# Performance work log

Hardware: AMD Instinct MI355X
Metric: run time of the kernel (lower is better)

The kernel has to match this reference:

```python
import jax, jax.numpy as jnp
import numpy as np

EPS = 1.1920929e-07  # torch nn.RMSNorm default eps = finfo(fp32).eps
H, NOPE, ROPE, VD = 16, 128, 64, 128
QKD = NOPE + ROPE


def rmsnorm(x, w):
    return x * jax.lax.rsqrt(jnp.mean(x * x, axis=-1, keepdims=True) + EPS) * w


def rope(x, cos, sin):
    # x: [B,S,h,D]; cos/sin broadcast to [B,S,h,D//2]; pairs are (even, odd) interleaved
    x2 = x.reshape(*x.shape[:-1], -1, 2)
    x0, x1 = x2[..., 0], x2[..., 1]
    r = x0 * cos - x1 * sin
    i = x0 * sin + x1 * cos
    return jnp.stack([r, i], axis=-1).reshape(x.shape)


def setup_inputs() -> dict:
    key = jax.random.key(0)
    ks = jax.random.split(key, 8)
    B, S, D = 2, 2048, 2048
    QR, KR = 1536, 512
    x = jax.random.normal(ks[0], (B, S, D), jnp.float32)
    # RoPE table: theta=10000, rope dim 64 -> 32 frequencies
    pos = np.arange(S)[:, None]
    inv = 1.0 / (10000.0 ** (np.arange(0, ROPE, 2) / ROPE))[None, :]
    ang = pos * inv
    freqs_cos = jnp.asarray(np.cos(ang), jnp.float32)
    freqs_sin = jnp.asarray(np.sin(ang), jnp.float32)

    def w(k, out_dim, in_dim):
        return jax.random.normal(k, (out_dim, in_dim), jnp.float32) / np.sqrt(in_dim)

    return {
        "x": x,
        "freqs_cos": freqs_cos,
        "freqs_sin": freqs_sin,
        "Wq_down": w(ks[1], QR, D),
        "q_norm_w": jnp.ones((QR,), jnp.float32),
        "Wq_up": w(ks[2], H * QKD, QR),
        "Wkv_down": w(ks[3], ROPE + KR, D),
        "kv_norm_w": jnp.ones((KR,), jnp.float32),
        "Wkv_up": w(ks[4], H * (VD + NOPE), KR),
        "Wo": w(ks[5], D, H * VD),
        "bo": jnp.zeros((D,), jnp.float32),
        "start_pos": 0,
    }


def reference(x, freqs_cos, freqs_sin, Wq_down, q_norm_w, Wq_up, Wkv_down, kv_norm_w, Wkv_up, Wo, bo, start_pos):
    B, S, D = x.shape
    cos = freqs_cos[None, :, None, :]
    sin = freqs_sin[None, :, None, :]
    # low-rank Q path: down -> RMSNorm -> up
    q = rmsnorm(x @ Wq_down.T, q_norm_w) @ Wq_up.T
    q = q.reshape(B, S, H, QKD)
    q_nope, q_rope = q[..., :NOPE], q[..., NOPE:]
    q_rope = rope(q_rope, cos, sin)
    q = jnp.concatenate([q_nope, q_rope], axis=-1)  # [B,S,H,QKD]
    # low-rank KV path: shared rope part + latent kv
    kv = x @ Wkv_down.T
    k_rope, c_kv = kv[..., :ROPE], kv[..., ROPE:]
    k_rope = rope(k_rope[:, :, None, :], cos, sin)  # [B,S,1,ROPE]
    kv = rmsnorm(c_kv, kv_norm_w) @ Wkv_up.T
    kv = kv.reshape(B, S, H, NOPE + VD)
    k_nope, v = kv[..., :NOPE], kv[..., NOPE:]
    k = jnp.concatenate([k_nope, jnp.broadcast_to(k_rope, (B, S, H, ROPE))], axis=-1)
    # causal SDPA (start_pos=0 prefill: cache slice equals fresh K/V)
    scale = 1.0 / np.sqrt(QKD)
    scores = jnp.einsum("bqhd,bkhd->bhqk", q, k) * scale
    mask = jnp.tril(jnp.ones((S, S), bool))
    scores = jnp.where(mask, scores, -jnp.inf)
    attn = jax.nn.softmax(scores, axis=-1)
    o = jnp.einsum("bhqk,bkhd->bqhd", attn, v).reshape(B, S, H * VD)
    return o @ Wo.T + bo
```

## Files before the change

### kernel.cpp

```cpp
#include <hip/hip_runtime.h>
#include <hip/hip_bf16.h>
#include <stdint.h>


typedef short bf16x8 __attribute__((ext_vector_type(8)));
typedef float f32x4  __attribute__((ext_vector_type(4)));
typedef unsigned int u32;

#define RMS_EPS 1.1920929e-07f
#define SCALE_L2E 0.10411931095f

__device__ __forceinline__ unsigned short f2b(float f) {
  union { float f; uint32_t u; } c; c.f = f;
  uint32_t u = c.u;
  return (unsigned short)((u + 0x7FFFu + ((u >> 16) & 1u)) >> 16);
}
__device__ __forceinline__ float b2f(short s) {
  union { uint32_t u; float f; } c; c.u = ((uint32_t)(unsigned short)s) << 16;
  return c.f;
}
__device__ __forceinline__ u32 pk2(float a, float b) {
  union { __hip_bfloat162 h; u32 u; } cv;
  cv.h = __float22bfloat162_rn(float2{a, b});
  return cv.u;
// ... 143 lines not shown
        } else {
          o0 = v0; o1 = v1; o2 = v2; o3 = v3;
        }
        uint2 o;
        o.x = pk2(o0 * SCALE_L2E, o1 * SCALE_L2E);
        o.y = pk2(o2 * SCALE_L2E, o3 * SCALE_L2E);
        *(uint2*)(qb + ((size_t)((b * 16 + h) * 2048 + s)) * 192 + d0) = o;
      }
    }
  } else {
    short* kb = (short*)Cv;
    short* vT = aux;
    int h = col0 >> 8;
    if ((col0 & 128) == 0) {
#pragma unroll
      for (int j = 0; j < 4; ++j) {
        int d = wn * 64 + j * 16 + l15;
#pragma unroll
        for (int i = 0; i < 4; ++i) {
          int rowb = row0 + wm * 64 + i * 16 + l4 * 4;
#pragma unroll
          for (int r = 0; r < 4; ++r) {
            int row = rowb + r;
            int b = row >> 11, s = row & 2047;
            kb[((size_t)((b * 16 + h) * 2048 + s)) * 128 + d] = (short)f2b(acc[i][j][r]);
          }
        }
      }
    } else {
#pragma unroll
      for (int j = 0; j < 4; ++j) {
        int dv = wn * 64 + j * 16 + l15;
#pragma unroll
        for (int i = 0; i < 4; ++i) {
          int s0 = row0 + wm * 64 + i * 16 + l4 * 4;
          int b = s0 >> 11, s = s0 & 2047;
          short4 o;
          o.x = (short)f2b(acc[i][j][0]);
          o.y = (short)f2b(acc[i][j][1]);
          o.z = (short)f2b(acc[i][j][2]);
          o.w = (short)f2b(acc[i][j][3]);
          *(short4*)(vT + ((size_t)((b * 16 + h) * 128 + dv)) * 2048 + s) = o;
        }
      }
    }
  }
}

template <int EPI>
__global__ __launch_bounds__(256) void gemm_bt(
    const short* __restrict__ A, const short* __restrict__ Bt,
    void* __restrict__ Cv, const float* __restrict__ bias,
    int K, int ldc,
    const float* __restrict__ fc, const float* __restrict__ fs,
    short* __restrict__ aux) {
  __shared__ __align__(16) short As[128 * 64];
  __shared__ __align__(16) short Bs[128 * 64];
  int nx = gridDim.x;
  int lin = blockIdx.y * nx + blockIdx.x;
  int cpx = (nx * gridDim.y) >> 3;
  int swz = (lin & 7) * cpx + (lin >> 3);
  int row0 = (swz / nx) * 128, col0 = (swz % nx) * 128;
  gemm_body<EPI>(As, Bs, row0, col0, A, Bt, Cv, bias, K, ldc, fc, fs, aux);
}

__global__ __launch_bounds__(256) void gemm_up(
    const short* __restrict__ qn, const short* __restrict__ wqu,
    short* __restrict__ q_b,
    const short* __restrict__ ckvn, const short* __restrict__ wkvu,
    short* __restrict__ k_b, short* __restrict__ vT,
    const float* __restrict__ fc, const float* __restrict__ fs) {
  __shared__ __align__(16) short As[128 * 64];
  __shared__ __align__(16) short Bs[128 * 64];
  int bb = blockIdx.x;
  if (bb < 768) {
    int cpx = 768 >> 3;
    int swz = (bb & 7) * cpx + (bb >> 3);
    int row0 = (swz / 24) * 128, col0 = (swz % 24) * 128;
    gemm_body<2>(As, Bs, row0, col0, qn, wqu, q_b, nullptr, 1536, 0, fc, fs, nullptr);
  } else {
    int bb2 = bb - 768;
    int cpx = 1024 >> 3;
    int swz = (bb2 & 7) * cpx + (bb2 >> 3);
    int row0 = (swz / 32) * 128, col0 = (swz % 32) * 128;
    gemm_body<3>(As, Bs, row0, col0, ckvn, wkvu, k_b, nullptr, 512, 0, nullptr, nullptr, vT);
  }
}

template <int W>
__device__ __forceinline__ void rms_body(
    const short* __restrict__ in, const float* __restrict__ wgt,
    short* __restrict__ out, int ld_in, int blk) {
  constexpr int NC = W / 512;
  int row = blk * 4 + (threadIdx.x >> 6);
  int lane = threadIdx.x & 63;
  const short* x = in + (size_t)row * ld_in + lane * 8;
  float vals[NC * 8];
  float ss = 0.f;
#pragma unroll
  for (int c = 0; c < NC; ++c) {
    bf16x8 v = *(const bf16x8*)(x + c * 512);
#pragma unroll
    for (int k = 0; k < 8; ++k) {
      float f = b2f(v[k]);
      vals[c * 8 + k] = f; ss += f * f;
    }
  }
#pragma unroll
  for (int off = 32; off > 0; off >>= 1) ss += __shfl_xor(ss, off);
  float rs = rsqrtf(ss / (float)W + RMS_EPS);
  short* o = out + (size_t)row * W + lane * 8;
#pragma unroll
  for (int c = 0; c < NC; ++c) {
    const float4* wp = (const float4*)(wgt + c * 512 + lane * 8);
    float4 w0 = wp[0], w1 = wp[1];
    ushort4 lo, hi;
    lo.x = f2b(vals[c * 8 + 0] * rs * w0.x);
    lo.y = f2b(vals[c * 8 + 1] * rs * w0.y);
    lo.z = f2b(vals[c * 8 + 2] * rs * w0.z);
    lo.w = f2b(vals[c * 8 + 3] * rs * w0.w);
    hi.x = f2b(vals[c * 8 + 4] * rs * w1.x);
    hi.y = f2b(vals[c * 8 + 5] * rs * w1.y);
    hi.z = f2b(vals[c * 8 + 6] * rs * w1.z);
    hi.w = f2b(vals[c * 8 + 7] * rs * w1.w);
    *(ushort4*)(o + c * 512) = lo;
    *(ushort4*)(o + c * 512 + 4) = hi;
  }
}

__global__ __launch_bounds__(256) void norm_krope_kernel(
    const short* __restrict__ c1,
    const float* __restrict__ qnw, short* __restrict__ qn,
    const float* __restrict__ kvnw, short* __restrict__ ckvn,
    const float* __restrict__ fc, const float* __restrict__ fs,
    short* __restrict__ kr) {
  int bb = blockIdx.x;
  if (bb < 1024) {
    rms_body<1536>(c1, qnw, qn, 2176, bb);
  } else if (bb < 2048) {
    rms_body<512>(c1 + 1600, kvnw, ckvn, 2176, bb - 1024);
  } else {
    int idx = (bb - 2048) * 256 + threadIdx.x;
    int i = idx & 31;
    int s = (idx >> 5) & 2047;
    int b = idx >> 16;
    const short* row = c1 + (size_t)(b * 2048 + s) * 2176 + 1536 + 2 * i;
    float x0 = b2f(row[0]), x1 = b2f(row[1]);
    float c = fc[s * 32 + i], sn = fs[s * 32 + i];
    uint32_t pk = (uint32_t)f2b(x0 * c - x1 * sn) | ((uint32_t)f2b(x0 * sn + x1 * c) << 16);
    *(uint32_t*)(kr + ((size_t)(b * 2048 + s)) * 64 + 2 * i) = pk;
  }
}

__global__ __launch_bounds__(256, 2) void attn_kernel(
    const short* __restrict__ qb, const short* __restrict__ kb,
    const short* __restrict__ kr, const short* __restrict__ vtb,
    short* __restrict__ ob) {
  __shared__ __align__(16) short Ks[64 * 196];
  __shared__ __align__(16) short Vs[128 * 70];
  int bid = blockIdx.x;
  int xcd = bid & 7, kk2 = bid >> 3;
  int bh = xcd * 4 + (kk2 >> 4);
  int qx = kk2 & 15;
  int b = bh >> 4, h = bh & 15;
  int t = threadIdx.x, lane = t & 63, w = t >> 6;
  int l15 = lane & 15, l4 = lane >> 4;
  const short* Kbh = kb + (size_t)bh * 2048 * 128;
  const short* krb = kr + (size_t)b * 2048 * 64;
  const short* Vbh = vtb + (size_t)bh * 128 * 2048;

  int kn_r = t >> 4, kn_c = (t & 15) * 8;
  int kr_r = t >> 3, kr_c = (t & 7) * 8;
  int v_d = t >> 3, v_c = (t & 7) * 8;

  int sA = (l15 + ((l4 & 1) << 5)) << 2;
  int sB = sA + (16 << 2);
  bool chi = (l4 >> 1) != 0;

  for (int half = 0; half < 2; ++half) {
    int qt = half ? (31 - qx) : qx;
    int q0 = qt * 64;
    const short* Qbase = qb + ((size_t)bh * 2048 + q0 + w * 16) * 192;
    bf16x8 qf[6];
#pragma unroll
    for (int kk = 0; kk < 6; ++kk)
      qf[kk] = *(const bf16x8*)(Qbase + (size_t)l15 * 192 + kk * 32 + l4 * 8);
    f32x4 oaccT[8] = {};
    float m_i = -1e30f, l_i = 0.f;
    int qcol = q0 + w * 16 + l15;
    int kend = q0 + 64;

    bf16x8 pn0, pn1, pn2, pn3, pr0, pr1, pv0, pv1, pv2, pv3;
    pn0 = *(const bf16x8*)(Kbh + (size_t)(kn_r) * 128 + kn_c);
    pn1 = *(const bf16x8*)(Kbh + (size_t)(kn_r + 16) * 128 + kn_c);
    pn2 = *(const bf16x8*)(Kbh + (size_t)(kn_r + 32) * 128 + kn_c);
    pn3 = *(const bf16x8*)(Kbh + (size_t)(kn_r + 48) * 128 + kn_c);
    pr0 = *(const bf16x8*)(krb + (size_t)(kr_r) * 64 + kr_c);
    pr1 = *(const bf16x8*)(krb + (size_t)(kr_r + 32) * 64 + kr_c);
    pv0 = *(const bf16x8*)(Vbh + (size_t)(v_d) * 2048 + v_c);
    pv1 = *(const bf16x8*)(Vbh + (size_t)(v_d + 32) * 2048 + v_c);
    pv2 = *(const bf16x8*)(Vbh + (size_t)(v_d + 64) * 2048 + v_c);
    pv3 = *(const bf16x8*)(Vbh + (size_t)(v_d + 96) * 2048 + v_c);

    for (int kt = 0; kt < kend; kt += 64) {
      *(bf16x8*)(Ks + (kn_r) * 196 + kn_c) = pn0;
      *(bf16x8*)(Ks + (kn_r + 16) * 196 + kn_c) = pn1;
      *(bf16x8*)(Ks + (kn_r + 32) * 196 + kn_c) = pn2;
      *(bf16x8*)(Ks + (kn_r + 48) * 196 + kn_c) = pn3;
      *(bf16x8*)(Ks + (kr_r) * 196 + 128 + kr_c) = pr0;
      *(bf16x8*)(Ks + (kr_r + 32) * 196 + 128 + kr_c) = pr1;
      *(bf16x8*)(Vs + (v_d) * 70 + v_c) = pv0;
      *(bf16x8*)(Vs + (v_d + 32) * 70 + v_c) = pv1;
      *(bf16x8*)(Vs + (v_d + 64) * 70 + v_c) = pv2;
      *(bf16x8*)(Vs + (v_d + 96) * 70 + v_c) = pv3;
      __syncthreads();
      if (kt + 64 < kend) {
        int k2 = kt + 64;
        pn0 = *(const bf16x8*)(Kbh + (size_t)(k2 + kn_r) * 128 + kn_c);
        pn1 = *(const bf16x8*)(Kbh + (size_t)(k2 + kn_r + 16) * 128 + kn_c);
        pn2 = *(const bf16x8*)(Kbh + (size_t)(k2 + kn_r + 32) * 128 + kn_c);
        pn3 = *(const bf16x8*)(Kbh + (size_t)(k2 + kn_r + 48) * 128 + kn_c);
        pr0 = *(const bf16x8*)(krb + (size_t)(k2 + kr_r) * 64 + kr_c);
        pr1 = *(const bf16x8*)(krb + (size_t)(k2 + kr_r + 32) * 64 + kr_c);
        pv0 = *(const bf16x8*)(Vbh + (size_t)(v_d) * 2048 + k2 + v_c);
        pv1 = *(const bf16x8*)(Vbh + (size_t)(v_d + 32) * 2048 + k2 + v_c);
        pv2 = *(const bf16x8*)(Vbh + (size_t)(v_d + 64) * 2048 + k2 + v_c);
        pv3 = *(const bf16x8*)(Vbh + (size_t)(v_d + 96) * 2048 + k2 + v_c);
      }

      f32x4 s[4] = {};
      __builtin_amdgcn_s_setprio(1);
#pragma unroll
      for (int kk = 0; kk < 6; ++kk) {
#pragma unroll
        for (int c = 0; c < 4; ++c) {
          bf16x8 kf = *(const bf16x8*)(Ks + (c * 16 + l15) * 196 + kk * 32 + l4 * 8);
          s[c] = __builtin_amdgcn_mfma_f32_16x16x32_bf16(kf, qf[kk], s[c], 0, 0, 0);
        }
      }
      __builtin_amdgcn_s_setprio(0);

      if (kt == q0) {
#pragma unroll
        for (int c = 0; c < 4; ++c)
#pragma unroll
          for (int r = 0; r < 4; ++r) {
            int k = kt + c * 16 + l4 * 4 + r;
            if (k > qcol) s[c][r] = -1e30f;
          }
      }
      float mx = fmaxf(fmaxf(fmaxf(s[0][0], s[0][1]), fmaxf(s[0][2], s[0][3])),
                       fmaxf(fmaxf(s[1][0], s[1][1]), fmaxf(s[1][2], s[1][3])));
      mx = fmaxf(mx, fmaxf(fmaxf(fmaxf(s[2][0], s[2][1]), fmaxf(s[2][2], s[2][3])),
                           fmaxf(fmaxf(s[3][0], s[3][1]), fmaxf(s[3][2], s[3][3]))));
      mx = fmaxf(mx, __shfl_xor(mx, 16));
      mx = fmaxf(mx, __shfl_xor(mx, 32));
      float newm = fmaxf(m_i, mx);
      float alpha = __builtin_amdgcn_exp2f(m_i - newm);
      float rs = 0.f;
#pragma unroll
      for (int c = 0; c < 4; ++c)
#pragma unroll
        for (int r = 0; r < 4; ++r) {
          float p = __builtin_amdgcn_exp2f(s[c][r] - newm);
          s[c][r] = p; rs += p;
        }
      rs += __shfl_xor(rs, 16);
      rs += __shfl_xor(rs, 32);
      l_i = l_i * alpha + rs;
      m_i = newm;
#pragma unroll
      for (int dt = 0; dt < 8; ++dt)
#pragma unroll
        for (int r = 0; r < 4; ++r) oaccT[dt][r] *= alpha;

      u32 pk00 = pk2(s[0][0], s[0][1]), pk01 = pk2(s[0][2], s[0][3]);
      u32 pk10 = pk2(s[1][0], s[1][1]), pk11 = pk2(s[1][2], s[1][3]);
      u32 pk20 = pk2(s[2][0], s[2][1]), pk21 = pk2(s[2][2], s[2][3]);
      u32 pk30 = pk2(s[3][0], s[3][1]), pk31 = pk2(s[3][2], s[3][3]);
      union { bf16x8 v; u32 u[4]; } P0, P1;
      {
        u32 a0 = __builtin_amdgcn_ds_bpermute(sA, (int)pk00);
        u32 a1 = __builtin_amdgcn_ds_bpermute(sA, (int)pk01);
        u32 a2 = __builtin_amdgcn_ds_bpermute(sB, (int)pk00);
        u32 a3 = __builtin_amdgcn_ds_bpermute(sB, (int)pk01);
        u32 b0 = __builtin_amdgcn_ds_bpermute(sA, (int)pk10);
        u32 b1 = __builtin_amdgcn_ds_bpermute(sA, (int)pk11);
        u32 b2 = __builtin_amdgcn_ds_bpermute(sB, (int)pk10);
        u32 b3 = __builtin_amdgcn_ds_bpermute(sB, (int)pk11);
        P0.u[0] = chi ? b0 : a0; P0.u[1] = chi ? b1 : a1;
        P0.u[2] = chi ? b2 : a2; P0.u[3] = chi ? b3 : a3;
      }
      {
        u32 a0 = __builtin_amdgcn_ds_bpermute(sA, (int)pk20);
        u32 a1 = __builtin_amdgcn_ds_bpermute(sA, (int)pk21);
        u32 a2 = __builtin_amdgcn_ds_bpermute(sB, (int)pk20);
        u32 a3 = __builtin_amdgcn_ds_bpermute(sB, (int)pk21);
        u32 b0 = __builtin_amdgcn_ds_bpermute(sA, (int)pk30);
        u32 b1 = __builtin_amdgcn_ds_bpermute(sA, (int)pk31);
        u32 b2 = __builtin_amdgcn_ds_bpermute(sB, (int)pk30);
        u32 b3 = __builtin_amdgcn_ds_bpermute(sB, (int)pk31);
        P1.u[0] = chi ? b0 : a0; P1.u[1] = chi ? b1 : a1;
        P1.u[2] = chi ? b2 : a2; P1.u[3] = chi ? b3 : a3;
      }

      __builtin_amdgcn_s_setprio(1);
#pragma unroll
      for (int dt = 0; dt < 8; ++dt) {
        bf16x8 vf0 = *(const bf16x8*)(Vs + (dt * 16 + l15) * 70 + l4 * 8);
        bf16x8 vf1 = *(const bf16x8*)(Vs + (dt * 16 + l15) * 70 + 32 + l4 * 8);
        oaccT[dt] = __builtin_amdgcn_mfma_f32_16x16x32_bf16(vf0, P0.v, oaccT[dt], 0, 0, 0);
        oaccT[dt] = __builtin_amdgcn_mfma_f32_16x16x32_bf16(vf1, P1.v, oaccT[dt], 0, 0, 0);
      }
      __builtin_amdgcn_s_setprio(0);
      __syncthreads();
    }
    float inv = 1.0f / l_i;
    short* dst = ob + ((size_t)(b * 2048 + qcol)) * 2048 + h * 128;
#pragma unroll
    for (int dt = 0; dt < 8; ++dt) {
      uint2 o;
      o.x = pk2(oaccT[dt][0] * inv, oaccT[dt][1] * inv);
      o.y = pk2(oaccT[dt][2] * inv, oaccT[dt][3] * inv);
      *(uint2*)(dst + dt * 16 + l4 * 4) = o;
    }
  }
}

extern "C" void kernel_launch(void* const* d_in, const int* in_sizes, int n_in,
                              void* d_out, int out_size, void* d_ws, size_t ws_size,
                              hipStream_t stream) {
  const float* x    = (const float*)d_in[0];
  const float* fcos = (const float*)d_in[1];
  const float* fsin = (const float*)d_in[2];
  const float* Wqd  = (const float*)d_in[3];
  const float* qnw  = (const float*)d_in[4];
  const float* Wqu  = (const float*)d_in[5];
  const float* Wkvd = (const float*)d_in[6];
  const float* kvnw = (const float*)d_in[7];
  const float* Wkvu = (const float*)d_in[8];
  const float* Wo   = (const float*)d_in[9];
  const float* bo   = (const float*)d_in[10];
  float* out = (float*)d_out;
  char* ws = (char*)d_ws;

  short* x_bf  = (short*)(ws + 0);
  short* w_cat = (short*)(ws + 16777216);
  short* w_qu  = (short*)(ws + 25690112);
  short* w_kvu = (short*)(ws + 35127296);
  short* w_o   = (short*)(ws + 39321600);
  short* c1    = (short*)(ws + 47710208);
  short* qn    = (short*)(ws + 65536000);
  short* ckvn  = (short*)(ws + 78118912);
  short* q_b   = (short*)(ws + 82313216);
  short* k_b   = (short*)(ws + 107479040);
  short* vT    = (short*)(ws + 132644864);
  short* o_bf  = (short*)(ws + 149422080);
  short* kr    = (short*)(ws + 166199296);

  f2bf_all_kernel<<<23296, 256, 0, stream>>>(x, x_bf, Wqd, w_cat, Wqu, w_qu,
                                             Wkvu, w_kvu, Wo, w_o,
                                             Wkvd, w_cat + 1536 * 2048);

  gemm_bt<1><<<dim3(17, 32), 256, 0, stream>>>(x_bf, w_cat, c1, nullptr, 2048, 2176,
                                               nullptr, nullptr, nullptr);
  norm_krope_kernel<<<2560, 256, 0, stream>>>(c1, qnw, qn, kvnw, ckvn,
                                              fcos, fsin, kr);

  gemm_up<<<1792, 256, 0, stream>>>(qn, w_qu, q_b, ckvn, w_kvu, k_b, vT,
                                    fcos, fsin);

  attn_kernel<<<512, 256, 0, stream>>>(q_b, k_b, kr, vT, o_bf);

  gemm_bt<0><<<dim3(16, 32), 256, 0, stream>>>(o_bf, w_o, out, bo, 2048, 2048,
                                               nullptr, nullptr, nullptr);
}
```

Baseline: 336.6 us.

## Split attention KV range across two blocks with a separate combine kernel

Each query-tile pair is now handled by two blocks, each covering half of the causal KV range and writing an unnormalized bf16 partial output along with its running max and sum. A new combine kernel merges the two partials with log-sum-exp weights and writes the normalized output. This doubles the attention grid to 1024 blocks to improve CU occupancy and load balance. It costs an extra kernel launch, extra global traffic for the partials, and some precision loss from storing unnormalized partials in bf16.

```diff
diff --git a/kernel.cpp b/kernel.cpp
--- a/kernel.cpp
+++ b/kernel.cpp
@@ -322,18 +322,18 @@
 __global__ __launch_bounds__(256, 2) void attn_kernel(
     const short* __restrict__ qb, const short* __restrict__ kb,
     const short* __restrict__ kr, const short* __restrict__ vtb,
-    short* __restrict__ ob) {
+    short* __restrict__ po, float* __restrict__ pml) {
   __shared__ __align__(16) short Ks[64 * 196];
   __shared__ __align__(16) short Vs[128 * 70];
   int bid = blockIdx.x;
-  int xcd = bid & 7, kk2 = bid >> 3;
-  int bh = xcd * 4 + (kk2 >> 4);
-  int qx = kk2 & 15;
-  int b = bh >> 4, h = bh & 15;
+  int xcd = bid & 7, rest = bid >> 3;
+  int bh = xcd * 4 + (rest >> 5);
+  int idx = rest & 31;
+  int p = idx >> 1, j = idx & 1;
   int t = threadIdx.x, lane = t & 63, w = t >> 6;
   int l15 = lane & 15, l4 = lane >> 4;
   const short* Kbh = kb + (size_t)bh * 2048 * 128;
-  const short* krb = kr + (size_t)b * 2048 * 64;
+  const short* krb = kr + (size_t)(bh >> 4) * 2048 * 64;
   const short* Vbh = vtb + (size_t)bh * 128 * 2048;
 
   int kn_r = t >> 4, kn_c = (t & 15) * 8;
@@ -345,8 +345,11 @@
   bool chi = (l4 >> 1) != 0;
 
   for (int half = 0; half < 2; ++half) {
-    int qt = half ? (31 - qx) : qx;
+    int qt = half ? (31 - p) : p;
     int q0 = qt * 64;
+    int n = qt + 1;
+    int lo = j * ((n + 1) >> 1);
+    int hi = j ? n : ((n + 1) >> 1);
     const short* Qbase = qb + ((size_t)bh * 2048 + q0 + w * 16) * 192;
     bf16x8 qf[6];
 #pragma unroll
@@ -355,142 +358,181 @@
     f32x4 oaccT[8] = {};
     float m_i = -1e30f, l_i = 0.f;
     int qcol = q0 + w * 16 + l15;
-    int kend = q0 + 64;
-
-    bf16x8 pn0, pn1, pn2, pn3, pr0, pr1, pv0, pv1, pv2, pv3;
-    pn0 = *(const bf16x8*)(Kbh + (size_t)(kn_r) * 128 + kn_c);
-    pn1 = *(const bf16x8*)(Kbh + (size_t)(kn_r + 16) * 128 + kn_c);
-    pn2 = *(const bf16x8*)(Kbh + (size_t)(kn_r + 32) * 128 + kn_c);
-    pn3 = *(const bf16x8*)(Kbh + (size_t)(kn_r + 48) * 128 + kn_c);
-    pr0 = *(const bf16x8*)(krb + (size_t)(kr_r) * 64 + kr_c);
-    pr1 = *(const bf16x8*)(krb + (size_t)(kr_r + 32) * 64 + kr_c);
-    pv0 = *(const bf16x8*)(Vbh + (size_t)(v_d) * 2048 + v_c);
-    pv1 = *(const bf16x8*)(Vbh + (size_t)(v_d + 32) * 2048 + v_c);
-    pv2 = *(const bf16x8*)(Vbh + (size_t)(v_d + 64) * 2048 + v_c);
-    pv3 = *(const bf16x8*)(Vbh + (size_t)(v_d + 96) * 2048 + v_c);
-
-    for (int kt = 0; kt < kend; kt += 64) {
-      *(bf16x8*)(Ks + (kn_r) * 196 + kn_c) = pn0;
-      *(bf16x8*)(Ks + (kn_r + 16) * 196 + kn_c) = pn1;
-      *(bf16x8*)(Ks + (kn_r + 32) * 196 + kn_c) = pn2;
-      *(bf16x8*)(Ks + (kn_r + 48) * 196 + kn_c) = pn3;
-      *(bf16x8*)(Ks + (kr_r) * 196 + 128 + kr_c) = pr0;
-      *(bf16x8*)(Ks + (kr_r + 32) * 196 + 128 + kr_c) = pr1;
-      *(bf16x8*)(Vs + (v_d) * 70 + v_c) = pv0;
-      *(bf16x8*)(Vs + (v_d + 32) * 70 + v_c) = pv1;
-      *(bf16x8*)(Vs + (v_d + 64) * 70 + v_c) = pv2;
-      *(bf16x8*)(Vs + (v_d + 96) * 70 + v_c) = pv3;
-      __syncthreads();
-      if (kt + 64 < kend) {
-        int k2 = kt + 64;
-        pn0 = *(const bf16x8*)(Kbh + (size_t)(k2 + kn_r) * 128 + kn_c);
-        pn1 = *(const bf16x8*)(Kbh + (size_t)(k2 + kn_r + 16) * 128 + kn_c);
-        pn2 = *(const bf16x8*)(Kbh + (size_t)(k2 + kn_r + 32) * 128 + kn_c);
-        pn3 = *(const bf16x8*)(Kbh + (size_t)(k2 + kn_r + 48) * 128 + kn_c);
-        pr0 = *(const bf16x8*)(krb + (size_t)(k2 + kr_r) * 64 + kr_c);
-        pr1 = *(const bf16x8*)(krb + (size_t)(k2 + kr_r + 32) * 64 + kr_c);
-        pv0 = *(const bf16x8*)(Vbh + (size_t)(v_d) * 2048 + k2 + v_c);
-        pv1 = *(const bf16x8*)(Vbh + (size_t)(v_d + 32) * 2048 + k2 + v_c);
-        pv2 = *(const bf16x8*)(Vbh + (size_t)(v_d + 64) * 2048 + k2 + v_c);
-        pv3 = *(const bf16x8*)(Vbh + (size_t)(v_d + 96) * 2048 + k2 + v_c);
-      }
-
-      f32x4 s[4] = {};
-      __builtin_amdgcn_s_setprio(1);
-#pragma unroll
-      for (int kk = 0; kk < 6; ++kk) {
-#pragma unroll
-        for (int c = 0; c < 4; ++c) {
-          bf16x8 kf = *(const bf16x8*)(Ks + (c * 16 + l15) * 196 + kk * 32 + l4 * 8);
-          s[c] = __builtin_amdgcn_mfma_f32_16x16x32_bf16(kf, qf[kk], s[c], 0, 0, 0);
-        }
-      }
-      __builtin_amdgcn_s_setprio(0);
-
-      if (kt == q0) {
+
+    if (lo < hi) {
+      bf16x8 pn0, pn1, pn2, pn3, pr0, pr1, pv0, pv1, pv2, pv3;
+      int k0 = lo * 64;
+      pn0 = *(const bf16x8*)(Kbh + (size_t)(k0 + kn_r) * 128 + kn_c);
+      pn1 = *(const bf16x8*)(Kbh + (size_t)(k0 + kn_r + 16) * 128 + kn_c);
+      pn2 = *(const bf16x8*)(Kbh + (size_t)(k0 + kn_r + 32) * 128 + kn_c);
+      pn3 = *(const bf16x8*)(Kbh + (size_t)(k0 + kn_r + 48) * 128 + kn_c);
+      pr0 = *(const bf16x8*)(krb + (size_t)(k0 + kr_r) * 64 + kr_c);
+      pr1 = *(const bf16x8*)(krb + (size_t)(k0 + kr_r + 32) * 64 + kr_c);
+      pv0 = *(const bf16x8*)(Vbh + (size_t)(v_d) * 2048 + k0 + v_c);
+      pv1 = *(const bf16x8*)(Vbh + (size_t)(v_d + 32) * 2048 + k0 + v_c);
+      pv2 = *(const bf16x8*)(Vbh + (size_t)(v_d + 64) * 2048 + k0 + v_c);
+      pv3 = *(const bf16x8*)(Vbh + (size_t)(v_d + 96) * 2048 + k0 + v_c);
+
+      for (int kt = lo * 64; kt < hi * 64; kt += 64) {
+        *(bf16x8*)(Ks + (kn_r) * 196 + kn_c) = pn0;
+        *(bf16x8*)(Ks + (kn_r + 16) * 196 + kn_c) = pn1;
+        *(bf16x8*)(Ks + (kn_r + 32) * 196 + kn_c) = pn2;
+        *(bf16x8*)(Ks + (kn_r + 48) * 196 + kn_c) = pn3;
+        *(bf16x8*)(Ks + (kr_r) * 196 + 128 + kr_c) = pr0;
+        *(bf16x8*)(Ks + (kr_r + 32) * 196 + 128 + kr_c) = pr1;
+        *(bf16x8*)(Vs + (v_d) * 70 + v_c) = pv0;
+        *(bf16x8*)(Vs + (v_d + 32) * 70 + v_c) = pv1;
+        *(bf16x8*)(Vs + (v_d + 64) * 70 + v_c) = pv2;
+        *(bf16x8*)(Vs + (v_d + 96) * 70 + v_c) = pv3;
+        __syncthreads();
+        if (kt + 64 < hi * 64) {
+          int k2 = kt + 64;
+          pn0 = *(const bf16x8*)(Kbh + (size_t)(k2 + kn_r) * 128 + kn_c);
+          pn1 = *(const bf16x8*)(Kbh + (size_t)(k2 + kn_r + 16) * 128 + kn_c);
+          pn2 = *(const bf16x8*)(Kbh + (size_t)(k2 + kn_r + 32) * 128 + kn_c);
+          pn3 = *(const bf16x8*)(Kbh + (size_t)(k2 + kn_r + 48) * 128 + kn_c);
+          pr0 = *(const bf16x8*)(krb + (size_t)(k2 + kr_r) * 64 + kr_c);
+          pr1 = *(const bf16x8*)(krb + (size_t)(k2 + kr_r + 32) * 64 + kr_c);
+          pv0 = *(const bf16x8*)(Vbh + (size_t)(v_d) * 2048 + k2 + v_c);
+          pv1 = *(const bf16x8*)(Vbh + (size_t)(v_d + 32) * 2048 + k2 + v_c);
+          pv2 = *(const bf16x8*)(Vbh + (size_t)(v_d + 64) * 2048 + k2 + v_c);
+          pv3 = *(const bf16x8*)(Vbh + (size_t)(v_d + 96) * 2048 + k2 + v_c);
+        }
+
+        f32x4 s[4] = {};
+        __builtin_amdgcn_s_setprio(1);
+#pragma unroll
+        for (int kk = 0; kk < 6; ++kk) {
+#pragma unroll
+          for (int c = 0; c < 4; ++c) {
+            bf16x8 kf = *(const bf16x8*)(Ks + (c * 16 + l15) * 196 + kk * 32 + l4 * 8);
+            s[c] = __builtin_amdgcn_mfma_f32_16x16x32_bf16(kf, qf[kk], s[c], 0, 0, 0);
+          }
+        }
+        __builtin_amdgcn_s_setprio(0);
+
+        if (kt == q0) {
+#pragma unroll
+          for (int c = 0; c < 4; ++c)
+#pragma unroll
+            for (int r = 0; r < 4; ++r) {
+              int k = kt + c * 16 + l4 * 4 + r;
+              if (k > qcol) s[c][r] = -1e30f;
+            }
+        }
+        float mx = fmaxf(fmaxf(fmaxf(s[0][0], s[0][1]), fmaxf(s[0][2], s[0][3])),
+                         fmaxf(fmaxf(s[1][0], s[1][1]), fmaxf(s[1][2], s[1][3])));
+        mx = fmaxf(mx, fmaxf(fmaxf(fmaxf(s[2][0], s[2][1]), fmaxf(s[2][2], s[2][3])),
+                             fmaxf(fmaxf(s[3][0], s[3][1]), fmaxf(s[3][2], s[3][3]))));
+        mx = fmaxf(mx, __shfl_xor(mx, 16));
+        mx = fmaxf(mx, __shfl_xor(mx, 32));
+        float newm = fmaxf(m_i, mx);
+        float alpha = __builtin_amdgcn_exp2f(m_i - newm);
+        float rs = 0.f;
 #pragma unroll
         for (int c = 0; c < 4; ++c)
 #pragma unroll
           for (int r = 0; r < 4; ++r) {
-            int k = kt + c * 16 + l4 * 4 + r;
-            if (k > qcol) s[c][r] = -1e30f;
+            float pv = __builtin_amdgcn_exp2f(s[c][r] - newm);
+            s[c][r] = pv; rs += pv;
           }
-      }
-      float mx = fmaxf(fmaxf(fmaxf(s[0][0], s[0][1]), fmaxf(s[0][2], s[0][3])),
-                       fmaxf(fmaxf(s[1][0], s[1][1]), fmaxf(s[1][2], s[1][3])));
-      mx = fmaxf(mx, fmaxf(fmaxf(fmaxf(s[2][0], s[2][1]), fmaxf(s[2][2], s[2][3])),
-                           fmaxf(fmaxf(s[3][0], s[3][1]), fmaxf(s[3][2], s[3][3]))));
-      mx = fmaxf(mx, __shfl_xor(mx, 16));
-      mx = fmaxf(mx, __shfl_xor(mx, 32));
-      float newm = fmaxf(m_i, mx);
-      float alpha = __builtin_amdgcn_exp2f(m_i - newm);
-      float rs = 0.f;
-#pragma unroll
-      for (int c = 0; c < 4; ++c)
-#pragma unroll
-        for (int r = 0; r < 4; ++r) {
-          float p = __builtin_amdgcn_exp2f(s[c][r] - newm);
-          s[c][r] = p; rs += p;
-        }
-      rs += __shfl_xor(rs, 16);
-      rs += __shfl_xor(rs, 32);
-      l_i = l_i * alpha + rs;
-      m_i = newm;
-#pragma unroll
-      for (int dt = 0; dt < 8; ++dt)
-#pragma unroll
-        for (int r = 0; r < 4; ++r) oaccT[dt][r] *= alpha;
-
-      u32 pk00 = pk2(s[0][0], s[0][1]), pk01 = pk2(s[0][2], s[0][3]);
-      u32 pk10 = pk2(s[1][0], s[1][1]), pk11 = pk2(s[1][2], s[1][3]);
-      u32 pk20 = pk2(s[2][0], s[2][1]), pk21 = pk2(s[2][2], s[2][3]);
-      u32 pk30 = pk2(s[3][0], s[3][1]), pk31 = pk2(s[3][2], s[3][3]);
-      union { bf16x8 v; u32 u[4]; } P0, P1;
-      {
-        u32 a0 = __builtin_amdgcn_ds_bpermute(sA, (int)pk00);
-        u32 a1 = __builtin_amdgcn_ds_bpermute(sA, (int)pk01);
-        u32 a2 = __builtin_amdgcn_ds_bpermute(sB, (int)pk00);
-        u32 a3 = __builtin_amdgcn_ds_bpermute(sB, (int)pk01);
-        u32 b0 = __builtin_amdgcn_ds_bpermute(sA, (int)pk10);
-        u32 b1 = __builtin_amdgcn_ds_bpermute(sA, (int)pk11);
-        u32 b2 = __builtin_amdgcn_ds_bpermute(sB, (int)pk10);
-        u32 b3 = __builtin_amdgcn_ds_bpermute(sB, (int)pk11);
-        P0.u[0] = chi ? b0 : a0; P0.u[1] = chi ? b1 : a1;
-        P0.u[2] = chi ? b2 : a2; P0.u[3] = chi ? b3 : a3;
-      }
-      {
-        u32 a0 = __builtin_amdgcn_ds_bpermute(sA, (int)pk20);
-        u32 a1 = __builtin_amdgcn_ds_bpermute(sA, (int)pk21);
-        u32 a2 = __builtin_amdgcn_ds_bpermute(sB, (int)pk20);
-        u32 a3 = __builtin_amdgcn_ds_bpermute(sB, (int)pk21);
-        u32 b0 = __builtin_amdgcn_ds_bpermute(sA, (int)pk30);
-        u32 b1 = __builtin_amdgcn_ds_bpermute(sA, (int)pk31);
-        u32 b2 = __builtin_amdgcn_ds_bpermute(sB, (int)pk30);
-        u32 b3 = __builtin_amdgcn_ds_bpermute(sB, (int)pk31);
-        P1.u[0] = chi ? b0 : a0; P1.u[1] = chi ? b1 : a1;
-        P1.u[2] = chi ? b2 : a2; P1.u[3] = chi ? b3 : a3;
-      }
-
-      __builtin_amdgcn_s_setprio(1);
-#pragma unroll
-      for (int dt = 0; dt < 8; ++dt) {
-        bf16x8 vf0 = *(const bf16x8*)(Vs + (dt * 16 + l15) * 70 + l4 * 8);
-        bf16x8 vf1 = *(const bf16x8*)(Vs + (dt * 16 + l15) * 70 + 32 + l4 * 8);
-        oaccT[dt] = __builtin_amdgcn_mfma_f32_16x16x32_bf16(vf0, P0.v, oaccT[dt], 0, 0, 0);
-        oaccT[dt] = __builtin_amdgcn_mfma_f32_16x16x32_bf16(vf1, P1.v, oaccT[dt], 0, 0, 0);
-      }
-      __builtin_amdgcn_s_setprio(0);
-      __syncthreads();
-    }
-    float inv = 1.0f / l_i;
-    short* dst = ob + ((size_t)(b * 2048 + qcol)) * 2048 + h * 128;
+        rs += __shfl_xor(rs, 16);
+        rs += __shfl_xor(rs, 32);
+        l_i = l_i * alpha + rs;
+        m_i = newm;
+#pragma unroll
+        for (int dt = 0; dt < 8; ++dt)
+#pragma unroll
+          for (int r = 0; r < 4; ++r) oaccT[dt][r] *= alpha;
+
+        u32 pk00 = pk2(s[0][0], s[0][1]), pk01 = pk2(s[0][2], s[0][3]);
+        u32 pk10 = pk2(s[1][0], s[1][1]), pk11 = pk2(s[1][2], s[1][3]);
+        u32 pk20 = pk2(s[2][0], s[2][1]), pk21 = pk2(s[2][2], s[2][3]);
+        u32 pk30 = pk2(s[3][0], s[3][1]), pk31 = pk2(s[3][2], s[3][3]);
+        union { bf16x8 v; u32 u[4]; } P0, P1;
+        {
+          u32 a0 = __builtin_amdgcn_ds_bpermute(sA, (int)pk00);
+          u32 a1 = __builtin_amdgcn_ds_bpermute(sA, (int)pk01);
+          u32 a2 = __builtin_amdgcn_ds_bpermute(sB, (int)pk00);
+          u32 a3 = __builtin_amdgcn_ds_bpermute(sB, (int)pk01);
+          u32 b0 = __builtin_amdgcn_ds_bpermute(sA, (int)pk10);
+          u32 b1 = __builtin_amdgcn_ds_bpermute(sA, (int)pk11);
+          u32 b2 = __builtin_amdgcn_ds_bpermute(sB, (int)pk10);
+          u32 b3 = __builtin_amdgcn_ds_bpermute(sB, (int)pk11);
+          P0.u[0] = chi ? b0 : a0; P0.u[1] = chi ? b1 : a1;
+          P0.u[2] = chi ? b2 : a2; P0.u[3] = chi ? b3 : a3;
+        }
+        {
+          u32 a0 = __builtin_amdgcn_ds_bpermute(sA, (int)pk20);
+          u32 a1 = __builtin_amdgcn_ds_bpermute(sA, (int)pk21);
+          u32 a2 = __builtin_amdgcn_ds_bpermute(sB, (int)pk20);
+          u32 a3 = __builtin_amdgcn_ds_bpermute(sB, (int)pk21);
+          u32 b0 = __builtin_amdgcn_ds_bpermute(sA, (int)pk30);
+          u32 b1 = __builtin_amdgcn_ds_bpermute(sA, (int)pk31);
+          u32 b2 = __builtin_amdgcn_ds_bpermute(sB, (int)pk30);
+          u32 b3 = __builtin_amdgcn_ds_bpermute(sB, (int)pk31);
+          P1.u[0] = chi ? b0 : a0; P1.u[1] = chi ? b1 : a1;
+          P1.u[2] = chi ? b2 : a2; P1.u[3] = chi ? b3 : a3;
+        }
+
+        __builtin_amdgcn_s_setprio(1);
+#pragma unroll
+        for (int dt = 0; dt < 8; ++dt) {
+          bf16x8 vf0 = *(const bf16x8*)(Vs + (dt * 16 + l15) * 70 + l4 * 8);
+          bf16x8 vf1 = *(const bf16x8*)(Vs + (dt * 16 + l15) * 70 + 32 + l4 * 8);
+          oaccT[dt] = __builtin_amdgcn_mfma_f32_16x16x32_bf16(vf0, P0.v, oaccT[dt], 0, 0, 0);
+          oaccT[dt] = __builtin_amdgcn_mfma_f32_16x16x32_bf16(vf1, P1.v, oaccT[dt], 0, 0, 0);
+        }
+        __builtin_amdgcn_s_setprio(0);
+        __syncthreads();
+      }
+    }
+    size_t pidx = ((size_t)bh * 32 + qt) * 2 + j;
+    short* dst = po + pidx * 8192 + (size_t)(w * 16 + l15) * 128;
 #pragma unroll
     for (int dt = 0; dt < 8; ++dt) {
       uint2 o;
-      o.x = pk2(oaccT[dt][0] * inv, oaccT[dt][1] * inv);
-      o.y = pk2(oaccT[dt][2] * inv, oaccT[dt][3] * inv);
+      o.x = pk2(oaccT[dt][0], oaccT[dt][1]);
+      o.y = pk2(oaccT[dt][2], oaccT[dt][3]);
       *(uint2*)(dst + dt * 16 + l4 * 4) = o;
     }
+    if (l4 == 0) {
+      float2 ml = {m_i, l_i};
+      *(float2*)(pml + pidx * 128 + (w * 16 + l15) * 2) = ml;
+    }
+  }
+}
+
+__global__ __launch_bounds__(256) void attn_combine_kernel(
+    const short* __restrict__ po, const float* __restrict__ pml,
+    short* __restrict__ ob) {
+  int bid = blockIdx.x;
+  int bh = bid >> 5, qt = bid & 31;
+  int b = bh >> 4, h = bh & 15;
+  int t = threadIdx.x;
+  int q = t >> 2, ds = (t & 3) * 32;
+  const float* ml0 = pml + ((size_t)bid * 2) * 128 + q * 2;
+  const float* ml1 = ml0 + 128;
+  float m0 = ml0[0], l0v = ml0[1];
+  float m1 = ml1[0], l1v = ml1[1];
+  float mm = fmaxf(m0, m1);
+  float w0 = __builtin_amdgcn_exp2f(m0 - mm);
+  float w1 = __builtin_amdgcn_exp2f(m1 - mm);
+  float inv = 1.0f / (l0v * w0 + l1v * w1);
+  w0 *= inv; w1 *= inv;
+  const short* p0 = po + ((size_t)bid * 2) * 8192 + q * 128 + ds;
+  const short* p1 = p0 + 8192;
+  short* dst = ob + ((size_t)(b * 2048 + qt * 64 + q)) * 2048 + h * 128 + ds;
+#pragma unroll
+  for (int c = 0; c < 4; ++c) {
+    bf16x8 a = *(const bf16x8*)(p0 + c * 8);
+    bf16x8 bb = *(const bf16x8*)(p1 + c * 8);
+    union { bf16x8 v; u32 u[4]; } o;
+    o.u[0] = pk2(b2f(a[0]) * w0 + b2f(bb[0]) * w1, b2f(a[1]) * w0 + b2f(bb[1]) * w1);
+    o.u[1] = pk2(b2f(a[2]) * w0 + b2f(bb[2]) * w1, b2f(a[3]) * w0 + b2f(bb[3]) * w1);
+    o.u[2] = pk2(b2f(a[4]) * w0 + b2f(bb[4]) * w1, b2f(a[5]) * w0 + b2f(bb[5]) * w1);
+    o.u[3] = pk2(b2f(a[6]) * w0 + b2f(bb[6]) * w1, b2f(a[7]) * w0 + b2f(bb[7]) * w1);
+    *(bf16x8*)(dst + c * 8) = o.v;
   }
 }
 
@@ -524,6 +566,8 @@
   short* vT    = (short*)(ws + 132644864);
   short* o_bf  = (short*)(ws + 149422080);
   short* kr    = (short*)(ws + 166199296);
+  short* po    = (short*)(ws + 166723584);
+  float* pml   = (float*)(ws + 200278016);
 
   f2bf_all_kernel<<<23296, 256, 0, stream>>>(x, x_bf, Wqd, w_cat, Wqu, w_qu,
                                              Wkvu, w_kvu, Wo, w_o,
@@ -537,7 +581,8 @@
   gemm_up<<<1792, 256, 0, stream>>>(qn, w_qu, q_b, ckvn, w_kvu, k_b, vT,
                                     fcos, fsin);
 
-  attn_kernel<<<512, 256, 0, stream>>>(q_b, k_b, kr, vT, o_bf);
+  attn_kernel<<<1024, 256, 0, stream>>>(q_b, k_b, kr, vT, po, pml);
+  attn_combine_kernel<<<1024, 256, 0, stream>>>(po, pml, o_bf);
 
   gemm_bt<0><<<dim3(16, 32), 256, 0, stream>>>(o_bf, w_o, out, bo, 2048, 2048,
                                                nullptr, nullptr, nullptr);
```

Result: slower. 356.7 us (+6.0%).

## Share K/V tile loads between paired causal query tiles in attention

Applied to the files above, without the earlier changes.

The attention kernel used to process its two query tiles (qx and 31-qx) one after another, streaming K/V from global memory once per tile. It now keeps both tiles' Q fragments and accumulators live at the same time and walks K/V only once. Each staged tile feeds the long query tile, and also the short one while it is still inside its causal range. This roughly halves K/V global loads and barrier rounds per block, but doubles the accumulator and Q register footprint, which risks spills or lower occupancy under launch_bounds(256,2).

```diff
diff --git a/kernel.cpp b/kernel.cpp
--- a/kernel.cpp
+++ b/kernel.cpp
@@ -319,6 +319,97 @@
   }
 }
 
+__device__ __forceinline__ void attn_step(
+    const short* Ks, const short* Vs, const bf16x8 (&qf)[6],
+    f32x4 (&oaccT)[8], float& m_i, float& l_i,
+    int kt, int q0, int qcol, int l15, int l4, int sA, int sB, bool chi) {
+  f32x4 s[4] = {};
+  __builtin_amdgcn_s_setprio(1);
+#pragma unroll
+  for (int kk = 0; kk < 6; ++kk) {
+#pragma unroll
+    for (int c = 0; c < 4; ++c) {
+      bf16x8 kf = *(const bf16x8*)(Ks + (c * 16 + l15) * 196 + kk * 32 + l4 * 8);
+      s[c] = __builtin_amdgcn_mfma_f32_16x16x32_bf16(kf, qf[kk], s[c], 0, 0, 0);
+    }
+  }
+  __builtin_amdgcn_s_setprio(0);
+
+  if (kt == q0) {
+#pragma unroll
+    for (int c = 0; c < 4; ++c)
+#pragma unroll
+      for (int r = 0; r < 4; ++r) {
+        int k = kt + c * 16 + l4 * 4 + r;
+        if (k > qcol) s[c][r] = -1e30f;
+      }
+  }
+  float mx = fmaxf(fmaxf(fmaxf(s[0][0], s[0][1]), fmaxf(s[0][2], s[0][3])),
+                   fmaxf(fmaxf(s[1][0], s[1][1]), fmaxf(s[1][2], s[1][3])));
+  mx = fmaxf(mx, fmaxf(fmaxf(fmaxf(s[2][0], s[2][1]), fmaxf(s[2][2], s[2][3])),
+                       fmaxf(fmaxf(s[3][0], s[3][1]), fmaxf(s[3][2], s[3][3]))));
+  mx = fmaxf(mx, __shfl_xor(mx, 16));
+  mx = fmaxf(mx, __shfl_xor(mx, 32));
+  float newm = fmaxf(m_i, mx);
+  float alpha = __builtin_amdgcn_exp2f(m_i - newm);
+  float rs = 0.f;
+#pragma unroll
+  for (int c = 0; c < 4; ++c)
+#pragma unroll
+    for (int r = 0; r < 4; ++r) {
+      float p = __builtin_amdgcn_exp2f(s[c][r] - newm);
+      s[c][r] = p; rs += p;
+    }
+  rs += __shfl_xor(rs, 16);
+  rs += __shfl_xor(rs, 32);
+  l_i = l_i * alpha + rs;
+  m_i = newm;
+#pragma unroll
+  for (int dt = 0; dt < 8; ++dt)
+#pragma unroll
+    for (int r = 0; r < 4; ++r) oaccT[dt][r] *= alpha;
+
+  u32 pk00 = pk2(s[0][0], s[0][1]), pk01 = pk2(s[0][2], s[0][3]);
+  u32 pk10 = pk2(s[1][0], s[1][1]), pk11 = pk2(s[1][2], s[1][3]);
+  u32 pk20 = pk2(s[2][0], s[2][1]), pk21 = pk2(s[2][2], s[2][3]);
+  u32 pk30 = pk2(s[3][0], s[3][1]), pk31 = pk2(s[3][2], s[3][3]);
+  union { bf16x8 v; u32 u[4]; } P0, P1;
+  {
+    u32 a0 = __builtin_amdgcn_ds_bpermute(sA, (int)pk00);
+    u32 a1 = __builtin_amdgcn_ds_bpermute(sA, (int)pk01);
+    u32 a2 = __builtin_amdgcn_ds_bpermute(sB, (int)pk00);
+    u32 a3 = __builtin_amdgcn_ds_bpermute(sB, (int)pk01);
+    u32 b0 = __builtin_amdgcn_ds_bpermute(sA, (int)pk10);
+    u32 b1 = __builtin_amdgcn_ds_bpermute(sA, (int)pk11);
+    u32 b2 = __builtin_amdgcn_ds_bpermute(sB, (int)pk10);
+    u32 b3 = __builtin_amdgcn_ds_bpermute(sB, (int)pk11);
+    P0.u[0] = chi ? b0 : a0; P0.u[1] = chi ? b1 : a1;
+    P0.u[2] = chi ? b2 : a2; P0.u[3] = chi ? b3 : a3;
+  }
+  {
+    u32 a0 = __builtin_amdgcn_ds_bpermute(sA, (int)pk20);
+    u32 a1 = __builtin_amdgcn_ds_bpermute(sA, (int)pk21);
+    u32 a2 = __builtin_amdgcn_ds_bpermute(sB, (int)pk20);
+    u32 a3 = __builtin_amdgcn_ds_bpermute(sB, (int)pk21);
+    u32 b0 = __builtin_amdgcn_ds_bpermute(sA, (int)pk30);
+    u32 b1 = __builtin_amdgcn_ds_bpermute(sA, (int)pk31);
+    u32 b2 = __builtin_amdgcn_ds_bpermute(sB, (int)pk30);
+    u32 b3 = __builtin_amdgcn_ds_bpermute(sB, (int)pk31);
+    P1.u[0] = chi ? b0 : a0; P1.u[1] = chi ? b1 : a1;
+    P1.u[2] = chi ? b2 : a2; P1.u[3] = chi ? b3 : a3;
+  }
+
+  __builtin_amdgcn_s_setprio(1);
+#pragma unroll
+  for (int dt = 0; dt < 8; ++dt) {
+    bf16x8 vf0 = *(const bf16x8*)(Vs + (dt * 16 + l15) * 70 + l4 * 8);
+    bf16x8 vf1 = *(const bf16x8*)(Vs + (dt * 16 + l15) * 70 + 32 + l4 * 8);
+    oaccT[dt] = __builtin_amdgcn_mfma_f32_16x16x32_bf16(vf0, P0.v, oaccT[dt], 0, 0, 0);
+    oaccT[dt] = __builtin_amdgcn_mfma_f32_16x16x32_bf16(vf1, P1.v, oaccT[dt], 0, 0, 0);
+  }
+  __builtin_amdgcn_s_setprio(0);
+}
+
 __global__ __launch_bounds__(256, 2) void attn_kernel(
     const short* __restrict__ qb, const short* __restrict__ kb,
     const short* __restrict__ kr, const short* __restrict__ vtb,
@@ -344,153 +435,78 @@
   int sB = sA + (16 << 2);
   bool chi = (l4 >> 1) != 0;
 
-  for (int half = 0; half < 2; ++half) {
-    int qt = half ? (31 - qx) : qx;
-    int q0 = qt * 64;
-    const short* Qbase = qb + ((size_t)bh * 2048 + q0 + w * 16) * 192;
-    bf16x8 qf[6];
-#pragma unroll
-    for (int kk = 0; kk < 6; ++kk)
-      qf[kk] = *(const bf16x8*)(Qbase + (size_t)l15 * 192 + kk * 32 + l4 * 8);
-    f32x4 oaccT[8] = {};
-    float m_i = -1e30f, l_i = 0.f;
-    int qcol = q0 + w * 16 + l15;
-    int kend = q0 + 64;
-
-    bf16x8 pn0, pn1, pn2, pn3, pr0, pr1, pv0, pv1, pv2, pv3;
-    pn0 = *(const bf16x8*)(Kbh + (size_t)(kn_r) * 128 + kn_c);
-    pn1 = *(const bf16x8*)(Kbh + (size_t)(kn_r + 16) * 128 + kn_c);
-    pn2 = *(const bf16x8*)(Kbh + (size_t)(kn_r + 32) * 128 + kn_c);
-    pn3 = *(const bf16x8*)(Kbh + (size_t)(kn_r + 48) * 128 + kn_c);
-    pr0 = *(const bf16x8*)(krb + (size_t)(kr_r) * 64 + kr_c);
-    pr1 = *(const bf16x8*)(krb + (size_t)(kr_r + 32) * 64 + kr_c);
-    pv0 = *(const bf16x8*)(Vbh + (size_t)(v_d) * 2048 + v_c);
-    pv1 = *(const bf16x8*)(Vbh + (size_t)(v_d + 32) * 2048 + v_c);
-    pv2 = *(const bf16x8*)(Vbh + (size_t)(v_d + 64) * 2048 + v_c);
-    pv3 = *(const bf16x8*)(Vbh + (size_t)(v_d + 96) * 2048 + v_c);
-
-    for (int kt = 0; kt < kend; kt += 64) {
-      *(bf16x8*)(Ks + (kn_r) * 196 + kn_c) = pn0;
-      *(bf16x8*)(Ks + (kn_r + 16) * 196 + kn_c) = pn1;
-      *(bf16x8*)(Ks + (kn_r + 32) * 196 + kn_c) = pn2;
-      *(bf16x8*)(Ks + (kn_r + 48) * 196 + kn_c) = pn3;
-      *(bf16x8*)(Ks + (kr_r) * 196 + 128 + kr_c) = pr0;
-      *(bf16x8*)(Ks + (kr_r + 32) * 196 + 128 + kr_c) = pr1;
-      *(bf16x8*)(Vs + (v_d) * 70 + v_c) = pv0;
-      *(bf16x8*)(Vs + (v_d + 32) * 70 + v_c) = pv1;
-      *(bf16x8*)(Vs + (v_d + 64) * 70 + v_c) = pv2;
-      *(bf16x8*)(Vs + (v_d + 96) * 70 + v_c) = pv3;
-      __syncthreads();
-      if (kt + 64 < kend) {
-        int k2 = kt + 64;
-        pn0 = *(const bf16x8*)(Kbh + (size_t)(k2 + kn_r) * 128 + kn_c);
-        pn1 = *(const bf16x8*)(Kbh + (size_t)(k2 + kn_r + 16) * 128 + kn_c);
-        pn2 = *(const bf16x8*)(Kbh + (size_t)(k2 + kn_r + 32) * 128 + kn_c);
-        pn3 = *(const bf16x8*)(Kbh + (size_t)(k2 + kn_r + 48) * 128 + kn_c);
-        pr0 = *(const bf16x8*)(krb + (size_t)(k2 + kr_r) * 64 + kr_c);
-        pr1 = *(const bf16x8*)(krb + (size_t)(k2 + kr_r + 32) * 64 + kr_c);
-        pv0 = *(const bf16x8*)(Vbh + (size_t)(v_d) * 2048 + k2 + v_c);
-        pv1 = *(const bf16x8*)(Vbh + (size_t)(v_d + 32) * 2048 + k2 + v_c);
-        pv2 = *(const bf16x8*)(Vbh + (size_t)(v_d + 64) * 2048 + k2 + v_c);
-        pv3 = *(const bf16x8*)(Vbh + (size_t)(v_d + 96) * 2048 + k2 + v_c);
-      }
-
-      f32x4 s[4] = {};
-      __builtin_amdgcn_s_setprio(1);
-#pragma unroll
-      for (int kk = 0; kk < 6; ++kk) {
-#pragma unroll
-        for (int c = 0; c < 4; ++c) {
-          bf16x8 kf = *(const bf16x8*)(Ks + (c * 16 + l15) * 196 + kk * 32 + l4 * 8);
-          s[c] = __builtin_amdgcn_mfma_f32_16x16x32_bf16(kf, qf[kk], s[c], 0, 0, 0);
-        }
-      }
-      __builtin_amdgcn_s_setprio(0);
-
-      if (kt == q0) {
-#pragma unroll
-        for (int c = 0; c < 4; ++c)
-#pragma unroll
-          for (int r = 0; r < 4; ++r) {
-            int k = kt + c * 16 + l4 * 4 + r;
-            if (k > qcol) s[c][r] = -1e30f;
-          }
-      }
-      float mx = fmaxf(fmaxf(fmaxf(s[0][0], s[0][1]), fmaxf(s[0][2], s[0][3])),
-                       fmaxf(fmaxf(s[1][0], s[1][1]), fmaxf(s[1][2], s[1][3])));
-      mx = fmaxf(mx, fmaxf(fmaxf(fmaxf(s[2][0], s[2][1]), fmaxf(s[2][2], s[2][3])),
-                           fmaxf(fmaxf(s[3][0], s[3][1]), fmaxf(s[3][2], s[3][3]))));
-      mx = fmaxf(mx, __shfl_xor(mx, 16));
-      mx = fmaxf(mx, __shfl_xor(mx, 32));
-      float newm = fmaxf(m_i, mx);
-      float alpha = __builtin_amdgcn_exp2f(m_i - newm);
-      float rs = 0.f;
-#pragma unroll
-      for (int c = 0; c < 4; ++c)
-#pragma unroll
-        for (int r = 0; r < 4; ++r) {
-          float p = __builtin_amdgcn_exp2f(s[c][r] - newm);
-          s[c][r] = p; rs += p;
-        }
-      rs += __shfl_xor(rs, 16);
-      rs += __shfl_xor(rs, 32);
-      l_i = l_i * alpha + rs;
-      m_i = newm;
-#pragma unroll
-      for (int dt = 0; dt < 8; ++dt)
-#pragma unroll
-        for (int r = 0; r < 4; ++r) oaccT[dt][r] *= alpha;
-
-      u32 pk00 = pk2(s[0][0], s[0][1]), pk01 = pk2(s[0][2], s[0][3]);
-      u32 pk10 = pk2(s[1][0], s[1][1]), pk11 = pk2(s[1][2], s[1][3]);
-      u32 pk20 = pk2(s[2][0], s[2][1]), pk21 = pk2(s[2][2], s[2][3]);
-      u32 pk30 = pk2(s[3][0], s[3][1]), pk31 = pk2(s[3][2], s[3][3]);
-      union { bf16x8 v; u32 u[4]; } P0, P1;
-      {
-        u32 a0 = __builtin_amdgcn_ds_bpermute(sA, (int)pk00);
-        u32 a1 = __builtin_amdgcn_ds_bpermute(sA, (int)pk01);
-        u32 a2 = __builtin_amdgcn_ds_bpermute(sB, (int)pk00);
-        u32 a3 = __builtin_amdgcn_ds_bpermute(sB, (int)pk01);
-        u32 b0 = __builtin_amdgcn_ds_bpermute(sA, (int)pk10);
-        u32 b1 = __builtin_amdgcn_ds_bpermute(sA, (int)pk11);
-        u32 b2 = __builtin_amdgcn_ds_bpermute(sB, (int)pk10);
-        u32 b3 = __builtin_amdgcn_ds_bpermute(sB, (int)pk11);
-        P0.u[0] = chi ? b0 : a0; P0.u[1] = chi ? b1 : a1;
-        P0.u[2] = chi ? b2 : a2; P0.u[3] = chi ? b3 : a3;
-      }
-      {
-        u32 a0 = __builtin_amdgcn_ds_bpermute(sA, (int)pk20);
-        u32 a1 = __builtin_amdgcn_ds_bpermute(sA, (int)pk21);
-        u32 a2 = __builtin_amdgcn_ds_bpermute(sB, (int)pk20);
-        u32 a3 = __builtin_amdgcn_ds_bpermute(sB, (int)pk21);
-        u32 b0 = __builtin_amdgcn_ds_bpermute(sA, (int)pk30);
-        u32 b1 = __builtin_amdgcn_ds_bpermute(sA, (int)pk31);
-        u32 b2 = __builtin_amdgcn_ds_bpermute(sB, (int)pk30);
-        u32 b3 = __builtin_amdgcn_ds_bpermute(sB, (int)pk31);
-        P1.u[0] = chi ? b0 : a0; P1.u[1] = chi ? b1 : a1;
-        P1.u[2] = chi ? b2 : a2; P1.u[3] = chi ? b3 : a3;
-      }
-
-      __builtin_amdgcn_s_setprio(1);
-#pragma unroll
-      for (int dt = 0; dt < 8; ++dt) {
-        bf16x8 vf0 = *(const bf16x8*)(Vs + (dt * 16 + l15) * 70 + l4 * 8);
-        bf16x8 vf1 = *(const bf16x8*)(Vs + (dt * 16 + l15) * 70 + 32 + l4 * 8);
-        oaccT[dt] = __builtin_amdgcn_mfma_f32_16x16x32_bf16(vf0, P0.v, oaccT[dt], 0, 0, 0);
-        oaccT[dt] = __builtin_amdgcn_mfma_f32_16x16x32_bf16(vf1, P1.v, oaccT[dt], 0, 0, 0);
-      }
-      __builtin_amdgcn_s_setprio(0);
-      __syncthreads();
-    }
-    float inv = 1.0f / l_i;
-    short* dst = ob + ((size_t)(b * 2048 + qcol)) * 2048 + h * 128;
-#pragma unroll
-    for (int dt = 0; dt < 8; ++dt) {
-      uint2 o;
-      o.x = pk2(oaccT[dt][0] * inv, oaccT[dt][1] * inv);
-      o.y = pk2(oaccT[dt][2] * inv, oaccT[dt][3] * inv);
-      *(uint2*)(dst + dt * 16 + l4 * 4) = o;
-    }
+  int q00 = qx * 64;
+  int q01 = (31 - qx) * 64;
+  const short* Qb0 = qb + ((size_t)bh * 2048 + q00 + w * 16) * 192;
+  const short* Qb1 = qb + ((size_t)bh * 2048 + q01 + w * 16) * 192;
+  bf16x8 qf0[6], qf1[6];
+#pragma unroll
+  for (int kk = 0; kk < 6; ++kk) {
+    qf0[kk] = *(const bf16x8*)(Qb0 + (size_t)l15 * 192 + kk * 32 + l4 * 8);
+    qf1[kk] = *(const bf16x8*)(Qb1 + (size_t)l15 * 192 + kk * 32 + l4 * 8);
+  }
+  f32x4 oa0[8] = {}, oa1[8] = {};
+  float m0 = -1e30f, l0 = 0.f, m1 = -1e30f, l1 = 0.f;
+  int qc0 = q00 + w * 16 + l15;
+  int qc1 = q01 + w * 16 + l15;
+  int kend = q01 + 64;
+
+  bf16x8 pn0, pn1, pn2, pn3, pr0, pr1, pv0, pv1, pv2, pv3;
+  pn0 = *(const bf16x8*)(Kbh + (size_t)(kn_r) * 128 + kn_c);
+  pn1 = *(const bf16x8*)(Kbh + (size_t)(kn_r + 16) * 128 + kn_c);
+  pn2 = *(const bf16x8*)(Kbh + (size_t)(kn_r + 32) * 128 + kn_c);
+  pn3 = *(const bf16x8*)(Kbh + (size_t)(kn_r + 48) * 128 + kn_c);
+  pr0 = *(const bf16x8*)(krb + (size_t)(kr_r) * 64 + kr_c);
+  pr1 = *(const bf16x8*)(krb + (size_t)(kr_r + 32) * 64 + kr_c);
+  pv0 = *(const bf16x8*)(Vbh + (size_t)(v_d) * 2048 + v_c);
+  pv1 = *(const bf16x8*)(Vbh + (size_t)(v_d + 32) * 2048 + v_c);
+  pv2 = *(const bf16x8*)(Vbh + (size_t)(v_d + 64) * 2048 + v_c);
+  pv3 = *(const bf16x8*)(Vbh + (size_t)(v_d + 96) * 2048 + v_c);
+
+  for (int kt = 0; kt < kend; kt += 64) {
+    *(bf16x8*)(Ks + (kn_r) * 196 + kn_c) = pn0;
+    *(bf16x8*)(Ks + (kn_r + 16) * 196 + kn_c) = pn1;
+    *(bf16x8*)(Ks + (kn_r + 32) * 196 + kn_c) = pn2;
+    *(bf16x8*)(Ks + (kn_r + 48) * 196 + kn_c) = pn3;
+    *(bf16x8*)(Ks + (kr_r) * 196 + 128 + kr_c) = pr0;
+    *(bf16x8*)(Ks + (kr_r + 32) * 196 + 128 + kr_c) = pr1;
+    *(bf16x8*)(Vs + (v_d) * 70 + v_c) = pv0;
+    *(bf16x8*)(Vs + (v_d + 32) * 70 + v_c) = pv1;
+    *(bf16x8*)(Vs + (v_d + 64) * 70 + v_c) = pv2;
+    *(bf16x8*)(Vs + (v_d + 96) * 70 + v_c) = pv3;
+    __syncthreads();
+    if (kt + 64 < kend) {
+      int k2 = kt + 64;
+      pn0 = *(const bf16x8*)(Kbh + (size_t)(k2 + kn_r) * 128 + kn_c);
+      pn1 = *(const bf16x8*)(Kbh + (size_t)(k2 + kn_r + 16) * 128 + kn_c);
+      pn2 = *(const bf16x8*)(Kbh + (size_t)(k2 + kn_r + 32) * 128 + kn_c);
+      pn3 = *(const bf16x8*)(Kbh + (size_t)(k2 + kn_r + 48) * 128 + kn_c);
+      pr0 = *(const bf16x8*)(krb + (size_t)(k2 + kr_r) * 64 + kr_c);
+      pr1 = *(const bf16x8*)(krb + (size_t)(k2 + kr_r + 32) * 64 + kr_c);
+      pv0 = *(const bf16x8*)(Vbh + (size_t)(v_d) * 2048 + k2 + v_c);
+      pv1 = *(const bf16x8*)(Vbh + (size_t)(v_d + 32) * 2048 + k2 + v_c);
+      pv2 = *(const bf16x8*)(Vbh + (size_t)(v_d + 64) * 2048 + k2 + v_c);
+      pv3 = *(const bf16x8*)(Vbh + (size_t)(v_d + 96) * 2048 + k2 + v_c);
+    }
+
+    attn_step(Ks, Vs, qf1, oa1, m1, l1, kt, q01, qc1, l15, l4, sA, sB, chi);
+    if (kt <= q00)
+      attn_step(Ks, Vs, qf0, oa0, m0, l0, kt, q00, qc0, l15, l4, sA, sB, chi);
+    __syncthreads();
+  }
+
+  float inv0 = 1.0f / l0, inv1 = 1.0f / l1;
+  short* dst0 = ob + ((size_t)(b * 2048 + qc0)) * 2048 + h * 128;
+  short* dst1 = ob + ((size_t)(b * 2048 + qc1)) * 2048 + h * 128;
+#pragma unroll
+  for (int dt = 0; dt < 8; ++dt) {
+    uint2 o0, o1;
+    o0.x = pk2(oa0[dt][0] * inv0, oa0[dt][1] * inv0);
+    o0.y = pk2(oa0[dt][2] * inv0, oa0[dt][3] * inv0);
+    o1.x = pk2(oa1[dt][0] * inv1, oa1[dt][1] * inv1);
+    o1.y = pk2(oa1[dt][2] * inv1, oa1[dt][3] * inv1);
+    *(uint2*)(dst0 + dt * 16 + l4 * 4) = o0;
+    *(uint2*)(dst1 + dt * 16 + l4 * 4) = o1;
   }
 }
 
```

Measured after the change: 557.6 us. 65.7% more time.
